# Performance work log

Measured on AMD Instinct MI355X. Metric: run time of the kernel, lower is better.

Reference implementation:

```python
import jax, jax.numpy as jnp
import numpy as np

N_BR, D, SD, RH, MH, UD, NOBS, B = 4, 256, 64, 64, 128, 16, 25, 32768
LN_EPS = 1e-5

def setup_inputs() -> dict:
    key = jax.random.key(0)
    ks = jax.random.split(key, 16)
    meas_in = D + SD
    rnn_in = RH + UD
    return {
        "z_dyn": jax.random.normal(ks[0], (B, D), jnp.float32),
        "z_static": jax.random.normal(ks[1], (B, SD), jnp.float32),
        "dt": jnp.ones((1,), jnp.float32),
        "ut": jax.random.normal(ks[2], (B, UD), jnp.float32),
        "gates": jax.random.normal(ks[3], (N_BR, D), jnp.float32) * 0.1,
        "W1": jax.random.normal(ks[4], (N_BR, MH, meas_in), jnp.float32) * (1.0 / np.sqrt(meas_in)),
        "b1": jnp.zeros((N_BR, MH), jnp.float32),
        "gamma": jnp.ones((N_BR, MH), jnp.float32),
        "beta": jnp.zeros((N_BR, MH), jnp.float32),
        "W2": jax.random.normal(ks[5], (N_BR, RH, MH), jnp.float32) * (1.0 / np.sqrt(MH)),
        "b2": jnp.zeros((N_BR, RH), jnp.float32),
        "lam_real": jnp.zeros((N_BR, RH), jnp.float32),
        "lam_imag": jax.random.normal(ks[6], (N_BR, RH), jnp.float32) * 0.1,
        "Bmat": jax.random.normal(ks[7], (N_BR, RH, rnn_in), jnp.float32) * (1.0 / np.sqrt(rnn_in)),
        "Wout": jax.random.normal(ks[8], (N_BR, D, RH), jnp.float32) * (1.0 / np.sqrt(RH)),
        "C": jax.random.normal(ks[9], (NOBS, D), jnp.float32) * (1.0 / np.sqrt(D)),
        "D": jax.random.normal(ks[10], (NOBS, UD), jnp.float32) * (1.0 / np.sqrt(UD)),
    }

def reference(z_dyn, z_static, dt, ut, gates, W1, b1, gamma, beta, W2, b2,
              lam_real, lam_imag, Bmat, Wout, C, D):
    ut_dt = ut * dt  # [B,u]
    n, Bsz = gates.shape[0], z_dyn.shape[0]
    # spectral gate per branch: [n,B,d]
    zg = z_dyn[None] * jax.nn.sigmoid(gates)[:, None, :]
    zs = jnp.broadcast_to(z_static[None], (n, Bsz, z_static.shape[-1]))
    x = jnp.concatenate([zg, zs], axis=-1)  # [n,B,meas_in]
    # measurement MLP: Linear -> LayerNorm -> GELU -> Linear
    h = jnp.einsum('nbi,nhi->nbh', x, W1) + b1[:, None, :]
    mu = h.mean(-1, keepdims=True)
    var = ((h - mu) ** 2).mean(-1, keepdims=True)
    h = (h - mu) / jnp.sqrt(var + LN_EPS) * gamma[:, None, :] + beta[:, None, :]
    h = jax.nn.gelu(h, approximate=False)
    g = jnp.einsum('nbh,noh->nbo', h, W2) + b2[:, None, :]  # [n,B,rnn_h]
    u_b = jnp.broadcast_to(ut_dt[None], (n, Bsz, ut_dt.shape[-1]))
    inp = jnp.concatenate([g, u_b], axis=-1)  # [n,B,rnn_h+u]
    b_inp = jnp.einsum('nbi,nhi->nbh', inp, Bmat)
    # complex recurrence step from h0 = 0 (as in forward())
    mag = jax.nn.sigmoid(lam_real) * 0.99
    lam_r = mag * jnp.cos(lam_imag)
    lam_i = mag * jnp.sin(lam_imag)
    h0r = jnp.zeros_like(b_inp)
    h0i = jnp.zeros_like(b_inp)
    h_real = h0r * lam_r[:, None, :] - h0i * lam_i[:, None, :] + b_inp
    # output projection per branch, summed over branches
    z_next = jnp.einsum('nbh,ndh->bd', h_real, Wout)
    yt = z_next @ C.T + ut_dt @ D.T
    return (z_next, yt)
```

## Files before the change

### kernel.cpp

```cpp
#include <hip/hip_runtime.h>
#include <hip/hip_bf16.h>

#define B_ROWS 32768
#define K1 320
#define N1 512
#define KH 512
#define K2 544
#define NP 384
#define LN_EPS 1e-5f

typedef __bf16 bf16;
using bf16x8 = __attribute__((ext_vector_type(8))) __bf16;
using f32x4  = __attribute__((ext_vector_type(4))) float;


__device__ __forceinline__ void gld_lds16(const bf16* g, bf16* l) {
  __builtin_amdgcn_global_load_lds((const __attribute__((address_space(1))) void*)g,
                                   (__attribute__((address_space(3))) void*)l,
                                   16, 0, 0);
}

__device__ __forceinline__ float gelu_exact(float x) {
  float s = x * 0.70710678118f;
  float a = fabsf(s);
  float t = __builtin_amdgcn_rcpf(fmaf(0.3275911f, a, 1.0f));
  float p = fmaf(fmaf(fmaf(fmaf(1.061405429f, t, -1.453152027f),
                           t, 1.421413741f), t, -0.284496736f), t, 0.254829592f) * t;
  float e = __expf(-s * s);
  float er = fmaf(-p, e, 1.0f);
  er = copysignf(er, s);
  return 0.5f * x * (1.0f + er);
}

__global__ __launch_bounds__(256) void prep_weights1(
    const float* __restrict__ gates, const float* __restrict__ W1,
    const float* __restrict__ Bmat,  const float* __restrict__ W2,
    const float* __restrict__ b2,    const float* __restrict__ Wout,
    const float* __restrict__ Cm,
    bf16* __restrict__ W1eff, float* __restrict__ Mtmp, float* __restrict__ cvec,
    float* __restrict__ CW)
{
  const int stride = gridDim.x * blockDim.x;
  const int id = blockIdx.x * blockDim.x + threadIdx.x;
  for (int i = id; i < 512 * 320; i += stride) {
    int col = i / 320;
    int k   = i - col * 320;
    float wv = W1[i];
    if (k < 256) {
      float g = gates[(col >> 7) * 256 + k];
      wv *= 1.f / (1.f + __expf(-g));
    }
    W1eff[i] = (bf16)wv;
  }
  for (int i = id; i < 4 * 64 * 128; i += stride) {
    int n = i >> 13, r = (i >> 7) & 63, h = i & 127;
    float s = 0.f;
    for (int j = 0; j < 64; ++j)
      s += Bmat[(n * 64 + r) * 80 + j] * W2[(n * 64 + j) * 128 + h];
    Mtmp[i] = s;
  }
  for (int i = id; i < 256; i += stride) {
    int n = i >> 6, r = i & 63;
    float s = 0.f;
    for (int j = 0; j < 64; ++j)
      s += Bmat[(n * 64 + r) * 80 + j] * b2[n * 64 + j];
    cvec[i] = s;
  }
  for (int i = id; i < 25 * 256; i += stride) {
    int o = i >> 8, nr = i & 255;
    float s = 0.f;
    for (int d = 0; d < 256; ++d)
      s += Cm[o * 256 + d] * Wout[((nr >> 6) * 256 + d) * 64 + (nr & 63)];
    CW[i] = s;
  }
}

__global__ __launch_bounds__(256) void prep_weights2(
    const float* __restrict__ Wout, const float* __restrict__ Bmat,
    const float* __restrict__ Mtmp, const float* __restrict__ cvec,
    const float* __restrict__ CW,   const float* __restrict__ Dm,
    bf16* __restrict__ Pext)
{
  const int stride = gridDim.x * blockDim.x;
  const int id = blockIdx.x * blockDim.x + threadIdx.x;
  for (int i = id; i < NP * 544; i += stride) {
    int dd = i / 544;
    int c  = i - dd * 544;
    float s = 0.f;
    if (dd < 281) {
      const bool isC = (dd >= 256);
      const int o = dd - 256;
      if (c < 512) {
        int n = c >> 7, h = c & 127;
        for (int r = 0; r < 64; ++r) {
          float wv = isC ? CW[(o * 4 + n) * 64 + r] : Wout[(n * 256 + dd) * 64 + r];
          s += wv * Mtmp[(n * 64 + r) * 128 + h];
        }
      } else if (c < 528) {
        int u = c - 512;
        for (int n = 0; n < 4; ++n)
          for (int r = 0; r < 64; ++r) {
            float wv = isC ? CW[(o * 4 + n) * 64 + r] : Wout[(n * 256 + dd) * 64 + r];
            s += wv * Bmat[(n * 64 + r) * 80 + 64 + u];
          }
        if (isC) s += Dm[o * 16 + u];
      } else if (c == 528) {
        for (int n = 0; n < 4; ++n)
          for (int r = 0; r < 64; ++r) {
            float wv = isC ? CW[(o * 4 + n) * 64 + r] : Wout[(n * 256 + dd) * 64 + r];
            s += wv * cvec[n * 64 + r];
          }
      }
    }
    Pext[i] = (bf16)s;
  }
}

__global__ __launch_bounds__(256) void gemm1_ln_gelu(
    const float* __restrict__ zdyn, const float* __restrict__ zst,
    const bf16* __restrict__ W,
    const float* __restrict__ b1, const float* __restrict__ gamma,
    const float* __restrict__ beta, bf16* __restrict__ H)
{
  __shared__ __align__(16) bf16 As[128 * 32];
  __shared__ __align__(16) bf16 Bs[128 * 32];
  __shared__ bf16 hs[128 * 130];
  __shared__ float sgam[128], sbet[128], sb1[128];

  const int t = threadIdx.x;
  const int lane = t & 63, w = t >> 6;
  const int rowBase = blockIdx.x * 128;
  const int colBase = blockIdx.y * 128;

  if (t < 128) {
    sgam[t] = gamma[colBase + t];
    sbet[t] = beta[colBase + t];
    sb1[t]  = b1[colBase + t];
  }

  const int s0 = t, s1 = t + 256;
  const int rA0 = s0 >> 2, pA0 = s0 & 3, qA0 = pA0 ^ ((rA0 >> 1) & 3);
  const int rA1 = s1 >> 2, pA1 = s1 & 3, qA1 = pA1 ^ ((rA1 >> 1) & 3);
  const float* pd0 = zdyn + (size_t)(rowBase + rA0) * 256 + qA0 * 8;
  const float* pd1 = zdyn + (size_t)(rowBase + rA1) * 256 + qA1 * 8;
  const float* ps0 = zst  + (size_t)(rowBase + rA0) * 64  + qA0 * 8;
  const float* ps1 = zst  + (size_t)(rowBase + rA1) * 64  + qA1 * 8;
  bf16* dA0 = As + rA0 * 32 + pA0 * 8;
  bf16* dA1 = As + rA1 * 32 + pA1 * 8;

  const bf16* gB0 = W + (size_t)(colBase + rA0) * K1 + qA0 * 8;
  const bf16* gB1 = W + (size_t)(colBase + rA1) * K1 + qA1 * 8;
  bf16* lB0 = Bs + w * 512;
  bf16* lB1 = Bs + 2048 + w * 512;

  f32x4 acc[4][4];
  #pragma unroll
  for (int i = 0; i < 4; ++i)
    #pragma unroll
    for (int j = 0; j < 4; ++j)
      #pragma unroll
      for (int r = 0; r < 4; ++r) acc[i][j][r] = 0.f;

  const int m16 = lane & 15, q = lane >> 4;
  const int wr = (w >> 1) * 64, wc = (w & 1) * 64;

  for (int it = 0; it < 10; ++it) {
    const float* p0 = (it < 8) ? pd0 + it * 32 : ps0 + (it - 8) * 32;
    const float* p1 = (it < 8) ? pd1 + it * 32 : ps1 + (it - 8) * 32;
    float4 a0 = *(const float4*)p0, a1 = *(const float4*)(p0 + 4);
    float4 b0 = *(const float4*)p1, b1v = *(const float4*)(p1 + 4);
    gld_lds16(gB0 + it * 32, lB0);
    gld_lds16(gB1 + it * 32, lB1);
    bf16x8 va, vb;
    va[0]=(bf16)a0.x; va[1]=(bf16)a0.y; va[2]=(bf16)a0.z; va[3]=(bf16)a0.w;
    va[4]=(bf16)a1.x; va[5]=(bf16)a1.y; va[6]=(bf16)a1.z; va[7]=(bf16)a1.w;
    vb[0]=(bf16)b0.x; vb[1]=(bf16)b0.y; vb[2]=(bf16)b0.z; vb[3]=(bf16)b0.w;
    vb[4]=(bf16)b1v.x; vb[5]=(bf16)b1v.y; vb[6]=(bf16)b1v.z; vb[7]=(bf16)b1v.w;
    *(bf16x8*)dA0 = va;
    *(bf16x8*)dA1 = vb;
    asm volatile("s_waitcnt vmcnt(0)" ::: "memory");
    __syncthreads();
    bf16x8 af[4], bfr[4];
    #pragma unroll
    for (int i = 0; i < 4; ++i) {
      int r = wr + i * 16 + m16;
      af[i]  = *(const bf16x8*)&As[r * 32 + ((q ^ ((r >> 1) & 3)) * 8)];
      int c = wc + i * 16 + m16;
      bfr[i] = *(const bf16x8*)&Bs[c * 32 + ((q ^ ((c >> 1) & 3)) * 8)];
    }
    #pragma unroll
    for (int i = 0; i < 4; ++i)
      #pragma unroll
      for (int j = 0; j < 4; ++j)
        acc[i][j] = __builtin_amdgcn_mfma_f32_16x16x32_bf16(af[i], bfr[j], acc[i][j], 0, 0, 0);
    __syncthreads();
  }

  #pragma unroll
  for (int j = 0; j < 4; ++j) {
    int col = wc + j * 16 + m16;
    float bb = sb1[col];
    #pragma unroll
    for (int i = 0; i < 4; ++i) {
      #pragma unroll
      for (int r = 0; r < 4; ++r) {
        int row = wr + i * 16 + q * 4 + r;
        hs[row * 130 + col] = (bf16)(acc[i][j][r] + bb);
      }
    }
  }
  __syncthreads();

  float* red  = (float*)As;
  float* red2 = (float*)Bs;
  float* smu_ = (float*)As + 512;
  float* srs_ = (float*)As + 768;
  {
    int row = t >> 1, c0 = (t & 1) * 64;
    float s = 0.f, s2 = 0.f;
    #pragma unroll
    for (int k = 0; k < 8; ++k) {
      bf16x8 hv = *(const bf16x8*)&hs[row * 130 + c0 + k * 8];
      #pragma unroll
      for (int j = 0; j < 8; ++j) { float v = (float)hv[j]; s += v; s2 = fmaf(v, v, s2); }
    }
    red[t] = s; red2[t] = s2;
  }
  __syncthreads();
  if (t < 128) {
    float ss = red[t * 2] + red[t * 2 + 1];
    float qq = red2[t * 2] + red2[t * 2 + 1];
    float mu = ss * 0.0078125f;
    float var = qq * 0.0078125f - mu * mu;
    smu_[t] = mu;
    srs_[t] = rsqrtf(fmaxf(var, 0.f) + LN_EPS);
  }
  __syncthreads();
  for (int e = t; e < 2048; e += 256) {
    int row = e >> 4, c8 = (e & 15) << 3;
    bf16x8 hv = *(const bf16x8*)&hs[row * 130 + c8];
    float mu = smu_[row], rs = srs_[row];
    bf16x8 ov;
    #pragma unroll
    for (int k = 0; k < 8; ++k) {
      float v = ((float)hv[k] - mu) * rs;
      v = fmaf(v, sgam[c8 + k], sbet[c8 + k]);
      ov[k] = (bf16)gelu_exact(v);
    }
    *(bf16x8*)&H[(size_t)(rowBase + row) * KH + colBase + c8] = ov;
  }
}

__global__ __launch_bounds__(256) void gemm2_z(
    const bf16* __restrict__ A, const bf16* __restrict__ Bm,
    const float* __restrict__ ut, const float* __restrict__ dtp,
    float* __restrict__ Z, float* __restrict__ yt)
{
  __shared__ __align__(16) bf16 As[128 * 32];
  __shared__ __align__(16) bf16 Bs[128 * 32];

  const int t = threadIdx.x;
  const int lane = t & 63, w = t >> 6;
  const int rowBase = blockIdx.x * 128;
  const int colBase = blockIdx.y * 128;
  const float dtv = dtp[0];

  const int s0 = t, s1 = t + 256;
  const int rA0 = s0 >> 2, pA0 = s0 & 3, qA0 = pA0 ^ ((rA0 >> 1) & 3);
  const int rA1 = s1 >> 2, pA1 = s1 & 3, qA1 = pA1 ^ ((rA1 >> 1) & 3);
  const bf16* gA0 = A + (size_t)(rowBase + rA0) * KH + qA0 * 8;
  const bf16* gA1 = A + (size_t)(rowBase + rA1) * KH + qA1 * 8;
  const bf16* gB0 = Bm + (size_t)(colBase + rA0) * K2 + qA0 * 8;
  const bf16* gB1 = Bm + (size_t)(colBase + rA1) * K2 + qA1 * 8;
  bf16* lA0 = As + w * 512;
  bf16* lA1 = As + 2048 + w * 512;
  bf16* lB0 = Bs + w * 512;
  bf16* lB1 = Bs + 2048 + w * 512;

  f32x4 acc[4][4];
  #pragma unroll
  for (int i = 0; i < 4; ++i)
    #pragma unroll
    for (int j = 0; j < 4; ++j)
      #pragma unroll
      for (int r = 0; r < 4; ++r) acc[i][j][r] = 0.f;

  const int m16 = lane & 15, q = lane >> 4;
  const int wr = (w >> 1) * 64, wc = (w & 1) * 64;

  for (int it = 0; it < 17; ++it) {
    if (it < 16) {
      gld_lds16(gA0 + it * 32, lA0);
      gld_lds16(gA1 + it * 32, lA1);
    } else {
      bf16x8 v0, v1;
      if (qA0 < 2) {
        const float* up = ut + (size_t)(rowBase + rA0) * 16 + qA0 * 8;
        float4 u0 = *(const float4*)up, u1 = *(const float4*)(up + 4);
        v0[0]=(bf16)(u0.x*dtv); v0[1]=(bf16)(u0.y*dtv); v0[2]=(bf16)(u0.z*dtv); v0[3]=(bf16)(u0.w*dtv);
        v0[4]=(bf16)(u1.x*dtv); v0[5]=(bf16)(u1.y*dtv); v0[6]=(bf16)(u1.z*dtv); v0[7]=(bf16)(u1.w*dtv);
      } else {
        #pragma unroll
        for (int k = 0; k < 8; ++k) v0[k] = (bf16)0.f;
        if (qA0 == 2) v0[0] = (bf16)1.f;
      }
      if (qA1 < 2) {
        const float* up = ut + (size_t)(rowBase + rA1) * 16 + qA1 * 8;
        float4 u0 = *(const float4*)up, u1 = *(const float4*)(up + 4);
        v1[0]=(bf16)(u0.x*dtv); v1[1]=(bf16)(u0.y*dtv); v1[2]=(bf16)(u0.z*dtv); v1[3]=(bf16)(u0.w*dtv);
        v1[4]=(bf16)(u1.x*dtv); v1[5]=(bf16)(u1.y*dtv); v1[6]=(bf16)(u1.z*dtv); v1[7]=(bf16)(u1.w*dtv);
      } else {
        #pragma unroll
        for (int k = 0; k < 8; ++k) v1[k] = (bf16)0.f;
        if (qA1 == 2) v1[0] = (bf16)1.f;
      }
      *(bf16x8*)&As[rA0 * 32 + pA0 * 8] = v0;
      *(bf16x8*)&As[rA1 * 32 + pA1 * 8] = v1;
    }
    gld_lds16(gB0 + it * 32, lB0);
    gld_lds16(gB1 + it * 32, lB1);
    asm volatile("s_waitcnt vmcnt(0)" ::: "memory");
    __syncthreads();
    bf16x8 af[4], bfr[4];
    #pragma unroll
    for (int i = 0; i < 4; ++i) {
      int r = wr + i * 16 + m16;
      af[i]  = *(const bf16x8*)&As[r * 32 + ((q ^ ((r >> 1) & 3)) * 8)];
      int c = wc + i * 16 + m16;
      bfr[i] = *(const bf16x8*)&Bs[c * 32 + ((q ^ ((c >> 1) & 3)) * 8)];
    }
    #pragma unroll
    for (int i = 0; i < 4; ++i)
      #pragma unroll
      for (int j = 0; j < 4; ++j)
        acc[i][j] = __builtin_amdgcn_mfma_f32_16x16x32_bf16(af[i], bfr[j], acc[i][j], 0, 0, 0);
    __syncthreads();
  }

  if (colBase < 256) {
    #pragma unroll
    for (int i = 0; i < 4; ++i)
      #pragma unroll
      for (int j = 0; j < 4; ++j) {
        int col = colBase + wc + j * 16 + m16;
        #pragma unroll
        for (int r = 0; r < 4; ++r) {
          int row = rowBase + wr + i * 16 + q * 4 + r;
          Z[(size_t)row * 256 + col] = acc[i][j][r];
        }
      }
  } else {
    #pragma unroll
    for (int i = 0; i < 4; ++i)
      #pragma unroll
      for (int j = 0; j < 4; ++j) {
        int col = colBase + wc + j * 16 + m16;
        if (col < 281) {
          #pragma unroll
          for (int r = 0; r < 4; ++r) {
            int row = rowBase + wr + i * 16 + q * 4 + r;
            yt[(size_t)row * 25 + (col - 256)] = acc[i][j][r];
          }
        }
      }
  }
}

extern "C" void kernel_launch(void* const* d_in, const int* in_sizes, int n_in,
                              void* d_out, int out_size, void* d_ws, size_t ws_size,
                              hipStream_t stream) {
  const float* zdyn  = (const float*)d_in[0];
  const float* zst   = (const float*)d_in[1];
  const float* dtp   = (const float*)d_in[2];
  const float* ut    = (const float*)d_in[3];
  const float* gates = (const float*)d_in[4];
  const float* W1    = (const float*)d_in[5];
  const float* b1    = (const float*)d_in[6];
  const float* gamma = (const float*)d_in[7];
  const float* beta  = (const float*)d_in[8];
  const float* W2    = (const float*)d_in[9];
  const float* b2    = (const float*)d_in[10];
  const float* Bmat  = (const float*)d_in[13];
  const float* Wout  = (const float*)d_in[14];
  const float* Cm    = (const float*)d_in[15];
  const float* Dm    = (const float*)d_in[16];

  char* ws = (char*)d_ws;
  bf16*  Hext  = (bf16*)(ws);
  bf16*  W1eff = (bf16*)(ws + 33554432);
  bf16*  Pext  = (bf16*)(ws + 33882112);
  float* Mtmp  = (float*)(ws + 34299904);
  float* cvec  = (float*)(ws + 34430976);
  float* CW    = (float*)(ws + 34432000);

  float* Z  = (float*)d_out;
  float* yt = Z + (size_t)B_ROWS * 256;

  hipLaunchKernelGGL(prep_weights1, dim3(128), dim3(256), 0, stream,
                     gates, W1, Bmat, W2, b2, Wout, Cm, W1eff, Mtmp, cvec, CW);
  hipLaunchKernelGGL(prep_weights2, dim3(256), dim3(256), 0, stream,
                     Wout, Bmat, Mtmp, cvec, CW, Dm, Pext);
  hipLaunchKernelGGL(gemm1_ln_gelu, dim3(256, 4), dim3(256), 0, stream,
                     zdyn, zst, W1eff, b1, gamma, beta, Hext);
  hipLaunchKernelGGL(gemm2_z, dim3(256, 3), dim3(256), 0, stream,
                     Hext, Pext, ut, dtp, Z, yt);
}
```

Before: 227.8 us.

## Fuse GEMM1+LayerNorm+GELU with GEMM2 into one kernel, keep hidden in LDS

Merges the two main GEMM kernels into a single 512-thread kernel per 128-row tile. It loops over the four branch chunks, computes GEMM1 with LayerNorm and GELU into shared memory, and immediately accumulates the second GEMM into registers. This removes the 32 MB bf16 hidden-activation round trip through global memory and one launch. Weights are pre-swizzled into MFMA fragment order so they can be read straight from global memory without LDS staging, but there are only 256 blocks and each block redundantly reloads z inputs for every chunk.

Measured after the change: 308.7 us. +35.5%, slower.

```diff
diff --git a/kernel.cpp b/kernel.cpp
--- a/kernel.cpp
+++ b/kernel.cpp
@@ -2,23 +2,12 @@
 #include <hip/hip_bf16.h>
 
 #define B_ROWS 32768
-#define K1 320
-#define N1 512
-#define KH 512
-#define K2 544
-#define NP 384
 #define LN_EPS 1e-5f
 
 typedef __bf16 bf16;
 using bf16x8 = __attribute__((ext_vector_type(8))) __bf16;
 using f32x4  = __attribute__((ext_vector_type(4))) float;
 
-
-__device__ __forceinline__ void gld_lds16(const bf16* g, bf16* l) {
-  __builtin_amdgcn_global_load_lds((const __attribute__((address_space(1))) void*)g,
-                                   (__attribute__((address_space(3))) void*)l,
-                                   16, 0, 0);
-}
 
 __device__ __forceinline__ float gelu_exact(float x) {
   float s = x * 0.70710678118f;
@@ -37,20 +26,21 @@
     const float* __restrict__ Bmat,  const float* __restrict__ W2,
     const float* __restrict__ b2,    const float* __restrict__ Wout,
     const float* __restrict__ Cm,
-    bf16* __restrict__ W1eff, float* __restrict__ Mtmp, float* __restrict__ cvec,
+    bf16* __restrict__ W1sw, float* __restrict__ Mtmp, float* __restrict__ cvec,
     float* __restrict__ CW)
 {
   const int stride = gridDim.x * blockDim.x;
   const int id = blockIdx.x * blockDim.x + threadIdx.x;
-  for (int i = id; i < 512 * 320; i += stride) {
-    int col = i / 320;
-    int k   = i - col * 320;
-    float wv = W1[i];
+  for (int o = id; o < 512 * 320; o += stride) {
+    int e = o & 7, m = (o >> 3) & 15, q2 = (o >> 7) & 3, rest = o >> 9;
+    int kk = rest % 10, G = rest / 10;
+    int n = G * 16 + m, k = kk * 32 + q2 * 8 + e;
+    float wv = W1[n * 320 + k];
     if (k < 256) {
-      float g = gates[(col >> 7) * 256 + k];
+      float g = gates[(n >> 7) * 256 + k];
       wv *= 1.f / (1.f + __expf(-g));
     }
-    W1eff[i] = (bf16)wv;
+    W1sw[o] = (bf16)wv;
   }
   for (int i = id; i < 4 * 64 * 128; i += stride) {
     int n = i >> 13, r = (i >> 7) & 63, h = i & 127;
@@ -79,291 +69,229 @@
     const float* __restrict__ Wout, const float* __restrict__ Bmat,
     const float* __restrict__ Mtmp, const float* __restrict__ cvec,
     const float* __restrict__ CW,   const float* __restrict__ Dm,
-    bf16* __restrict__ Pext)
+    bf16* __restrict__ Psw)
 {
   const int stride = gridDim.x * blockDim.x;
   const int id = blockIdx.x * blockDim.x + threadIdx.x;
-  for (int i = id; i < NP * 544; i += stride) {
-    int dd = i / 544;
-    int c  = i - dd * 544;
+  for (int o = id; o < 320 * 544; o += stride) {
+    int e = o & 7, m = (o >> 3) & 15, q2 = (o >> 7) & 3, rest = o >> 9;
+    int kk2 = rest % 17, G2 = rest / 17;
+    int dd = G2 * 16 + m, cc = kk2 * 32 + q2 * 8 + e;
     float s = 0.f;
     if (dd < 281) {
       const bool isC = (dd >= 256);
-      const int o = dd - 256;
-      if (c < 512) {
-        int n = c >> 7, h = c & 127;
+      const int oo = dd - 256;
+      if (cc < 512) {
+        int n = cc >> 7, h = cc & 127;
         for (int r = 0; r < 64; ++r) {
-          float wv = isC ? CW[(o * 4 + n) * 64 + r] : Wout[(n * 256 + dd) * 64 + r];
+          float wv = isC ? CW[(oo * 4 + n) * 64 + r] : Wout[(n * 256 + dd) * 64 + r];
           s += wv * Mtmp[(n * 64 + r) * 128 + h];
         }
-      } else if (c < 528) {
-        int u = c - 512;
+      } else if (cc < 528) {
+        int u = cc - 512;
         for (int n = 0; n < 4; ++n)
           for (int r = 0; r < 64; ++r) {
-            float wv = isC ? CW[(o * 4 + n) * 64 + r] : Wout[(n * 256 + dd) * 64 + r];
+            float wv = isC ? CW[(oo * 4 + n) * 64 + r] : Wout[(n * 256 + dd) * 64 + r];
             s += wv * Bmat[(n * 64 + r) * 80 + 64 + u];
           }
-        if (isC) s += Dm[o * 16 + u];
-      } else if (c == 528) {
+        if (isC) s += Dm[oo * 16 + u];
+      } else if (cc == 528) {
         for (int n = 0; n < 4; ++n)
           for (int r = 0; r < 64; ++r) {
-            float wv = isC ? CW[(o * 4 + n) * 64 + r] : Wout[(n * 256 + dd) * 64 + r];
+            float wv = isC ? CW[(oo * 4 + n) * 64 + r] : Wout[(n * 256 + dd) * 64 + r];
             s += wv * cvec[n * 64 + r];
           }
       }
     }
-    Pext[i] = (bf16)s;
-  }
-}
-
-__global__ __launch_bounds__(256) void gemm1_ln_gelu(
+    Psw[o] = (bf16)s;
+  }
+}
+
+__global__ __launch_bounds__(512, 2) void fused_main(
     const float* __restrict__ zdyn, const float* __restrict__ zst,
-    const bf16* __restrict__ W,
-    const float* __restrict__ b1, const float* __restrict__ gamma,
-    const float* __restrict__ beta, bf16* __restrict__ H)
+    const float* __restrict__ ut,   const float* __restrict__ dtp,
+    const bf16* __restrict__ W1sw,  const bf16* __restrict__ Psw,
+    const float* __restrict__ b1,   const float* __restrict__ gamma,
+    const float* __restrict__ beta,
+    float* __restrict__ Z, float* __restrict__ yt)
 {
-  __shared__ __align__(16) bf16 As[128 * 32];
-  __shared__ __align__(16) bf16 Bs[128 * 32];
-  __shared__ bf16 hs[128 * 130];
-  __shared__ float sgam[128], sbet[128], sb1[128];
+  __shared__ __align__(16) bf16 Hc[4 * 128 * 32];
+  __shared__ __align__(16) bf16 Ht[128 * 32];
+  __shared__ float sgam[512], sbet[512], sb1[512];
+  __shared__ float smu[128], srs[128];
 
   const int t = threadIdx.x;
-  const int lane = t & 63, w = t >> 6;
+  const int lane = t & 63, m16 = lane & 15, q = lane >> 4;
+  const int w = t >> 6, wrow = (w & 1) * 64, wcol = w >> 1;
   const int rowBase = blockIdx.x * 128;
-  const int colBase = blockIdx.y * 128;
-
-  if (t < 128) {
-    sgam[t] = gamma[colBase + t];
-    sbet[t] = beta[colBase + t];
-    sb1[t]  = b1[colBase + t];
-  }
-
-  const int s0 = t, s1 = t + 256;
-  const int rA0 = s0 >> 2, pA0 = s0 & 3, qA0 = pA0 ^ ((rA0 >> 1) & 3);
-  const int rA1 = s1 >> 2, pA1 = s1 & 3, qA1 = pA1 ^ ((rA1 >> 1) & 3);
-  const float* pd0 = zdyn + (size_t)(rowBase + rA0) * 256 + qA0 * 8;
-  const float* pd1 = zdyn + (size_t)(rowBase + rA1) * 256 + qA1 * 8;
-  const float* ps0 = zst  + (size_t)(rowBase + rA0) * 64  + qA0 * 8;
-  const float* ps1 = zst  + (size_t)(rowBase + rA1) * 64  + qA1 * 8;
-  bf16* dA0 = As + rA0 * 32 + pA0 * 8;
-  bf16* dA1 = As + rA1 * 32 + pA1 * 8;
-
-  const bf16* gB0 = W + (size_t)(colBase + rA0) * K1 + qA0 * 8;
-  const bf16* gB1 = W + (size_t)(colBase + rA1) * K1 + qA1 * 8;
-  bf16* lB0 = Bs + w * 512;
-  bf16* lB1 = Bs + 2048 + w * 512;
-
-  f32x4 acc[4][4];
+
+  sgam[t] = gamma[t]; sbet[t] = beta[t]; sb1[t] = b1[t];
+
+  {
+    const float dtv = dtp[0];
+    int r = t >> 2, pq = t & 3;
+    int lq = pq ^ ((r >> 1) & 3);
+    bf16x8 o;
+    #pragma unroll
+    for (int e = 0; e < 8; ++e) {
+      int ci = lq * 8 + e;
+      float v = (ci < 16) ? ut[(size_t)(rowBase + r) * 16 + ci] * dtv
+                          : (ci == 16 ? 1.f : 0.f);
+      o[e] = (bf16)v;
+    }
+    *(bf16x8*)&Ht[t * 8] = o;
+  }
+
+  f32x4 accZ[4][5];
   #pragma unroll
   for (int i = 0; i < 4; ++i)
     #pragma unroll
-    for (int j = 0; j < 4; ++j)
-      #pragma unroll
-      for (int r = 0; r < 4; ++r) acc[i][j][r] = 0.f;
-
-  const int m16 = lane & 15, q = lane >> 4;
-  const int wr = (w >> 1) * 64, wc = (w & 1) * 64;
-
-  for (int it = 0; it < 10; ++it) {
-    const float* p0 = (it < 8) ? pd0 + it * 32 : ps0 + (it - 8) * 32;
-    const float* p1 = (it < 8) ? pd1 + it * 32 : ps1 + (it - 8) * 32;
-    float4 a0 = *(const float4*)p0, a1 = *(const float4*)(p0 + 4);
-    float4 b0 = *(const float4*)p1, b1v = *(const float4*)(p1 + 4);
-    gld_lds16(gB0 + it * 32, lB0);
-    gld_lds16(gB1 + it * 32, lB1);
-    bf16x8 va, vb;
-    va[0]=(bf16)a0.x; va[1]=(bf16)a0.y; va[2]=(bf16)a0.z; va[3]=(bf16)a0.w;
-    va[4]=(bf16)a1.x; va[5]=(bf16)a1.y; va[6]=(bf16)a1.z; va[7]=(bf16)a1.w;
-    vb[0]=(bf16)b0.x; vb[1]=(bf16)b0.y; vb[2]=(bf16)b0.z; vb[3]=(bf16)b0.w;
-    vb[4]=(bf16)b1v.x; vb[5]=(bf16)b1v.y; vb[6]=(bf16)b1v.z; vb[7]=(bf16)b1v.w;
-    *(bf16x8*)dA0 = va;
-    *(bf16x8*)dA1 = vb;
-    asm volatile("s_waitcnt vmcnt(0)" ::: "memory");
+    for (int j = 0; j < 5; ++j)
+      #pragma unroll
+      for (int r = 0; r < 4; ++r) accZ[i][j][r] = 0.f;
+
+  #pragma unroll 1
+  for (int c = 0; c < 4; ++c) {
+    f32x4 acc1[4][2];
+    #pragma unroll
+    for (int i = 0; i < 4; ++i)
+      #pragma unroll
+      for (int j = 0; j < 2; ++j)
+        #pragma unroll
+        for (int r = 0; r < 4; ++r) acc1[i][j][r] = 0.f;
+
+    #pragma unroll
+    for (int kk = 0; kk < 10; ++kk) {
+      bf16x8 bfr[2];
+      #pragma unroll
+      for (int j = 0; j < 2; ++j) {
+        int G = c * 8 + wcol * 2 + j;
+        bfr[j] = *(const bf16x8*)&W1sw[(size_t)(((G * 10 + kk) * 4 + q) * 16 + m16) * 8];
+      }
+      bf16x8 af[4];
+      #pragma unroll
+      for (int i = 0; i < 4; ++i) {
+        int row = rowBase + wrow + i * 16 + m16;
+        const float* src = (kk < 8) ? &zdyn[(size_t)row * 256 + kk * 32 + q * 8]
+                                    : &zst[(size_t)row * 64 + (kk - 8) * 32 + q * 8];
+        float4 v0 = *(const float4*)src;
+        float4 v1 = *(const float4*)(src + 4);
+        af[i][0] = (bf16)v0.x; af[i][1] = (bf16)v0.y;
+        af[i][2] = (bf16)v0.z; af[i][3] = (bf16)v0.w;
+        af[i][4] = (bf16)v1.x; af[i][5] = (bf16)v1.y;
+        af[i][6] = (bf16)v1.z; af[i][7] = (bf16)v1.w;
+      }
+      #pragma unroll
+      for (int i = 0; i < 4; ++i)
+        #pragma unroll
+        for (int j = 0; j < 2; ++j)
+          acc1[i][j] = __builtin_amdgcn_mfma_f32_16x16x32_bf16(af[i], bfr[j], acc1[i][j], 0, 0, 0);
+    }
+
     __syncthreads();
-    bf16x8 af[4], bfr[4];
+    #pragma unroll
+    for (int j = 0; j < 2; ++j) {
+      int tc = j * 16 + m16;
+      float bb = sb1[c * 128 + wcol * 32 + tc];
+      int lq2 = tc >> 3, e2 = tc & 7;
+      #pragma unroll
+      for (int i = 0; i < 4; ++i)
+        #pragma unroll
+        for (int rr = 0; rr < 4; ++rr) {
+          int row = wrow + i * 16 + q * 4 + rr;
+          Hc[((wcol * 128 + row) * 4 + (lq2 ^ ((row >> 1) & 3))) * 8 + e2] =
+              (bf16)(acc1[i][j][rr] + bb);
+        }
+    }
+    __syncthreads();
+    if (t < 128) {
+      float s = 0.f, s2 = 0.f;
+      #pragma unroll
+      for (int tk = 0; tk < 4; ++tk)
+        #pragma unroll
+        for (int ch = 0; ch < 4; ++ch) {
+          bf16x8 hv = *(const bf16x8*)&Hc[((tk * 128 + t) * 4 + ch) * 8];
+          #pragma unroll
+          for (int e = 0; e < 8; ++e) { float v = (float)hv[e]; s += v; s2 = fmaf(v, v, s2); }
+        }
+      float mu = s * 0.0078125f;
+      float var = s2 * 0.0078125f - mu * mu;
+      smu[t] = mu;
+      srs[t] = rsqrtf(fmaxf(var, 0.f) + LN_EPS);
+    }
+    __syncthreads();
+    #pragma unroll
+    for (int a = 0; a < 4; ++a) {
+      int id = t + 512 * a;
+      int tk = id >> 9, rem = id & 511, r = rem >> 2, pq = rem & 3;
+      int lq = pq ^ ((r >> 1) & 3);
+      int gcol = c * 128 + tk * 32 + lq * 8;
+      bf16x8 hv = *(const bf16x8*)&Hc[id * 8];
+      float mu = smu[r], rs = srs[r];
+      bf16x8 ov;
+      #pragma unroll
+      for (int e = 0; e < 8; ++e) {
+        float v = ((float)hv[e] - mu) * rs;
+        v = fmaf(v, sgam[gcol + e], sbet[gcol + e]);
+        ov[e] = (bf16)gelu_exact(v);
+      }
+      *(bf16x8*)&Hc[id * 8] = ov;
+    }
+    __syncthreads();
+
+    #pragma unroll
+    for (int tk = 0; tk < 4; ++tk) {
+      int kk2 = c * 4 + tk;
+      bf16x8 af[4], bfr[5];
+      #pragma unroll
+      for (int i = 0; i < 4; ++i) {
+        int row = wrow + i * 16 + m16;
+        af[i] = *(const bf16x8*)&Hc[((tk * 128 + row) * 4 + (q ^ ((row >> 1) & 3))) * 8];
+      }
+      #pragma unroll
+      for (int j = 0; j < 5; ++j) {
+        int G2 = wcol * 5 + j;
+        bfr[j] = *(const bf16x8*)&Psw[(size_t)(((G2 * 17 + kk2) * 4 + q) * 16 + m16) * 8];
+      }
+      #pragma unroll
+      for (int i = 0; i < 4; ++i)
+        #pragma unroll
+        for (int j = 0; j < 5; ++j)
+          accZ[i][j] = __builtin_amdgcn_mfma_f32_16x16x32_bf16(af[i], bfr[j], accZ[i][j], 0, 0, 0);
+    }
+  }
+
+  {
+    bf16x8 af[4], bfr[5];
     #pragma unroll
     for (int i = 0; i < 4; ++i) {
-      int r = wr + i * 16 + m16;
-      af[i]  = *(const bf16x8*)&As[r * 32 + ((q ^ ((r >> 1) & 3)) * 8)];
-      int c = wc + i * 16 + m16;
-      bfr[i] = *(const bf16x8*)&Bs[c * 32 + ((q ^ ((c >> 1) & 3)) * 8)];
+      int row = wrow + i * 16 + m16;
+      af[i] = *(const bf16x8*)&Ht[(row * 4 + (q ^ ((row >> 1) & 3))) * 8];
+    }
+    #pragma unroll
+    for (int j = 0; j < 5; ++j) {
+      int G2 = wcol * 5 + j;
+      bfr[j] = *(const bf16x8*)&Psw[(size_t)(((G2 * 17 + 16) * 4 + q) * 16 + m16) * 8];
     }
     #pragma unroll
     for (int i = 0; i < 4; ++i)
       #pragma unroll
-      for (int j = 0; j < 4; ++j)
-        acc[i][j] = __builtin_amdgcn_mfma_f32_16x16x32_bf16(af[i], bfr[j], acc[i][j], 0, 0, 0);
-    __syncthreads();
-  }
-
-  #pragma unroll
-  for (int j = 0; j < 4; ++j) {
-    int col = wc + j * 16 + m16;
-    float bb = sb1[col];
-    #pragma unroll
-    for (int i = 0; i < 4; ++i) {
-      #pragma unroll
-      for (int r = 0; r < 4; ++r) {
-        int row = wr + i * 16 + q * 4 + r;
-        hs[row * 130 + col] = (bf16)(acc[i][j][r] + bb);
-      }
-    }
-  }
-  __syncthreads();
-
-  float* red  = (float*)As;
-  float* red2 = (float*)Bs;
-  float* smu_ = (float*)As + 512;
-  float* srs_ = (float*)As + 768;
-  {
-    int row = t >> 1, c0 = (t & 1) * 64;
-    float s = 0.f, s2 = 0.f;
-    #pragma unroll
-    for (int k = 0; k < 8; ++k) {
-      bf16x8 hv = *(const bf16x8*)&hs[row * 130 + c0 + k * 8];
-      #pragma unroll
-      for (int j = 0; j < 8; ++j) { float v = (float)hv[j]; s += v; s2 = fmaf(v, v, s2); }
-    }
-    red[t] = s; red2[t] = s2;
-  }
-  __syncthreads();
-  if (t < 128) {
-    float ss = red[t * 2] + red[t * 2 + 1];
-    float qq = red2[t * 2] + red2[t * 2 + 1];
-    float mu = ss * 0.0078125f;
-    float var = qq * 0.0078125f - mu * mu;
-    smu_[t] = mu;
-    srs_[t] = rsqrtf(fmaxf(var, 0.f) + LN_EPS);
-  }
-  __syncthreads();
-  for (int e = t; e < 2048; e += 256) {
-    int row = e >> 4, c8 = (e & 15) << 3;
-    bf16x8 hv = *(const bf16x8*)&hs[row * 130 + c8];
-    float mu = smu_[row], rs = srs_[row];
-    bf16x8 ov;
-    #pragma unroll
-    for (int k = 0; k < 8; ++k) {
-      float v = ((float)hv[k] - mu) * rs;
-      v = fmaf(v, sgam[c8 + k], sbet[c8 + k]);
-      ov[k] = (bf16)gelu_exact(v);
-    }
-    *(bf16x8*)&H[(size_t)(rowBase + row) * KH + colBase + c8] = ov;
-  }
-}
-
-__global__ __launch_bounds__(256) void gemm2_z(
-    const bf16* __restrict__ A, const bf16* __restrict__ Bm,
-    const float* __restrict__ ut, const float* __restrict__ dtp,
-    float* __restrict__ Z, float* __restrict__ yt)
-{
-  __shared__ __align__(16) bf16 As[128 * 32];
-  __shared__ __align__(16) bf16 Bs[128 * 32];
-
-  const int t = threadIdx.x;
-  const int lane = t & 63, w = t >> 6;
-  const int rowBase = blockIdx.x * 128;
-  const int colBase = blockIdx.y * 128;
-  const float dtv = dtp[0];
-
-  const int s0 = t, s1 = t + 256;
-  const int rA0 = s0 >> 2, pA0 = s0 & 3, qA0 = pA0 ^ ((rA0 >> 1) & 3);
-  const int rA1 = s1 >> 2, pA1 = s1 & 3, qA1 = pA1 ^ ((rA1 >> 1) & 3);
-  const bf16* gA0 = A + (size_t)(rowBase + rA0) * KH + qA0 * 8;
-  const bf16* gA1 = A + (size_t)(rowBase + rA1) * KH + qA1 * 8;
-  const bf16* gB0 = Bm + (size_t)(colBase + rA0) * K2 + qA0 * 8;
-  const bf16* gB1 = Bm + (size_t)(colBase + rA1) * K2 + qA1 * 8;
-  bf16* lA0 = As + w * 512;
-  bf16* lA1 = As + 2048 + w * 512;
-  bf16* lB0 = Bs + w * 512;
-  bf16* lB1 = Bs + 2048 + w * 512;
-
-  f32x4 acc[4][4];
+      for (int j = 0; j < 5; ++j)
+        accZ[i][j] = __builtin_amdgcn_mfma_f32_16x16x32_bf16(af[i], bfr[j], accZ[i][j], 0, 0, 0);
+  }
+
   #pragma unroll
   for (int i = 0; i < 4; ++i)
     #pragma unroll
-    for (int j = 0; j < 4; ++j)
-      #pragma unroll
-      for (int r = 0; r < 4; ++r) acc[i][j][r] = 0.f;
-
-  const int m16 = lane & 15, q = lane >> 4;
-  const int wr = (w >> 1) * 64, wc = (w & 1) * 64;
-
-  for (int it = 0; it < 17; ++it) {
-    if (it < 16) {
-      gld_lds16(gA0 + it * 32, lA0);
-      gld_lds16(gA1 + it * 32, lA1);
-    } else {
-      bf16x8 v0, v1;
-      if (qA0 < 2) {
-        const float* up = ut + (size_t)(rowBase + rA0) * 16 + qA0 * 8;
-        float4 u0 = *(const float4*)up, u1 = *(const float4*)(up + 4);
-        v0[0]=(bf16)(u0.x*dtv); v0[1]=(bf16)(u0.y*dtv); v0[2]=(bf16)(u0.z*dtv); v0[3]=(bf16)(u0.w*dtv);
-        v0[4]=(bf16)(u1.x*dtv); v0[5]=(bf16)(u1.y*dtv); v0[6]=(bf16)(u1.z*dtv); v0[7]=(bf16)(u1.w*dtv);
-      } else {
-        #pragma unroll
-        for (int k = 0; k < 8; ++k) v0[k] = (bf16)0.f;
-        if (qA0 == 2) v0[0] = (bf16)1.f;
-      }
-      if (qA1 < 2) {
-        const float* up = ut + (size_t)(rowBase + rA1) * 16 + qA1 * 8;
-        float4 u0 = *(const float4*)up, u1 = *(const float4*)(up + 4);
-        v1[0]=(bf16)(u0.x*dtv); v1[1]=(bf16)(u0.y*dtv); v1[2]=(bf16)(u0.z*dtv); v1[3]=(bf16)(u0.w*dtv);
-        v1[4]=(bf16)(u1.x*dtv); v1[5]=(bf16)(u1.y*dtv); v1[6]=(bf16)(u1.z*dtv); v1[7]=(bf16)(u1.w*dtv);
-      } else {
-        #pragma unroll
-        for (int k = 0; k < 8; ++k) v1[k] = (bf16)0.f;
-        if (qA1 == 2) v1[0] = (bf16)1.f;
-      }
-      *(bf16x8*)&As[rA0 * 32 + pA0 * 8] = v0;
-      *(bf16x8*)&As[rA1 * 32 + pA1 * 8] = v1;
-    }
-    gld_lds16(gB0 + it * 32, lB0);
-    gld_lds16(gB1 + it * 32, lB1);
-    asm volatile("s_waitcnt vmcnt(0)" ::: "memory");
-    __syncthreads();
-    bf16x8 af[4], bfr[4];
-    #pragma unroll
-    for (int i = 0; i < 4; ++i) {
-      int r = wr + i * 16 + m16;
-      af[i]  = *(const bf16x8*)&As[r * 32 + ((q ^ ((r >> 1) & 3)) * 8)];
-      int c = wc + i * 16 + m16;
-      bfr[i] = *(const bf16x8*)&Bs[c * 32 + ((q ^ ((c >> 1) & 3)) * 8)];
-    }
-    #pragma unroll
-    for (int i = 0; i < 4; ++i)
-      #pragma unroll
-      for (int j = 0; j < 4; ++j)
-        acc[i][j] = __builtin_amdgcn_mfma_f32_16x16x32_bf16(af[i], bfr[j], acc[i][j], 0, 0, 0);
-    __syncthreads();
-  }
-
-  if (colBase < 256) {
-    #pragma unroll
-    for (int i = 0; i < 4; ++i)
-      #pragma unroll
-      for (int j = 0; j < 4; ++j) {
-        int col = colBase + wc + j * 16 + m16;
-        #pragma unroll
-        for (int r = 0; r < 4; ++r) {
-          int row = rowBase + wr + i * 16 + q * 4 + r;
-          Z[(size_t)row * 256 + col] = acc[i][j][r];
-        }
-      }
-  } else {
-    #pragma unroll
-    for (int i = 0; i < 4; ++i)
-      #pragma unroll
-      for (int j = 0; j < 4; ++j) {
-        int col = colBase + wc + j * 16 + m16;
-        if (col < 281) {
-          #pragma unroll
-          for (int r = 0; r < 4; ++r) {
-            int row = rowBase + wr + i * 16 + q * 4 + r;
-            yt[(size_t)row * 25 + (col - 256)] = acc[i][j][r];
-          }
-        }
-      }
-  }
+    for (int j = 0; j < 5; ++j) {
+      int col = wcol * 80 + j * 16 + m16;
+      #pragma unroll
+      for (int rr = 0; rr < 4; ++rr) {
+        int row = rowBase + wrow + i * 16 + q * 4 + rr;
+        if (col < 256) Z[(size_t)row * 256 + col] = accZ[i][j][rr];
+        else if (col < 281) yt[(size_t)row * 25 + (col - 256)] = accZ[i][j][rr];
+      }
+    }
 }
 
 extern "C" void kernel_launch(void* const* d_in, const int* in_sizes, int n_in,
@@ -386,22 +314,19 @@
   const float* Dm    = (const float*)d_in[16];
 
   char* ws = (char*)d_ws;
-  bf16*  Hext  = (bf16*)(ws);
-  bf16*  W1eff = (bf16*)(ws + 33554432);
-  bf16*  Pext  = (bf16*)(ws + 33882112);
-  float* Mtmp  = (float*)(ws + 34299904);
-  float* cvec  = (float*)(ws + 34430976);
-  float* CW    = (float*)(ws + 34432000);
+  bf16*  W1sw = (bf16*)(ws);
+  bf16*  Psw  = (bf16*)(ws + 327680);
+  float* Mtmp = (float*)(ws + 675840);
+  float* cvec = (float*)(ws + 806912);
+  float* CW   = (float*)(ws + 807936);
 
   float* Z  = (float*)d_out;
   float* yt = Z + (size_t)B_ROWS * 256;
 
   hipLaunchKernelGGL(prep_weights1, dim3(128), dim3(256), 0, stream,
-                     gates, W1, Bmat, W2, b2, Wout, Cm, W1eff, Mtmp, cvec, CW);
+                     gates, W1, Bmat, W2, b2, Wout, Cm, W1sw, Mtmp, cvec, CW);
   hipLaunchKernelGGL(prep_weights2, dim3(256), dim3(256), 0, stream,
-                     Wout, Bmat, Mtmp, cvec, CW, Dm, Pext);
-  hipLaunchKernelGGL(gemm1_ln_gelu, dim3(256, 4), dim3(256), 0, stream,
-                     zdyn, zst, W1eff, b1, gamma, beta, Hext);
-  hipLaunchKernelGGL(gemm2_z, dim3(256, 3), dim3(256), 0, stream,
-                     Hext, Pext, ut, dtp, Z, yt);
-}
+                     Wout, Bmat, Mtmp, cvec, CW, Dm, Psw);
+  hipLaunchKernelGGL(fused_main, dim3(256), dim3(512), 0, stream,
+                     zdyn, zst, ut, dtp, W1sw, Psw, b1, gamma, beta, Z, yt);
+}
```
